# Performance work log

Measured on AMD Instinct MI355X. Metric: run time of the kernel, lower is better.

Reference implementation:

```python
import jax, jax.numpy as jnp
import numpy as np

NEG_SLOPE = 0.2

def setup_inputs() -> dict:
    key = jax.random.key(0)
    ks = jax.random.split(key, 6)
    N, C, H, E_DIM, E = 50000, 128, 64, 16, 800000
    x = jax.random.normal(ks[0], (N, C), dtype=jnp.float32)
    edge_index = jax.random.randint(ks[1], (2, E), 0, N, dtype=jnp.int64)
    edge_attr = jax.random.normal(ks[2], (E, E_DIM), dtype=jnp.float32)
    fc_w = jax.random.normal(ks[3], (H, C), dtype=jnp.float32) * (1.0 / np.sqrt(C))
    fc_b = jnp.zeros((H,), dtype=jnp.float32)
    att_w = jax.random.normal(ks[4], (H, 2 * H + E_DIM), dtype=jnp.float32) * (1.0 / np.sqrt(2 * H + E_DIM))
    att_b = jnp.zeros((H,), dtype=jnp.float32)
    return {"x": x, "edge_index": edge_index, "edge_attr": edge_attr,
            "fc_w": fc_w, "fc_b": fc_b, "att_w": att_w, "att_b": att_b}

def reference(x, edge_index, edge_attr, fc_w, fc_b, att_w, att_b):
    # Node projection: h = fc(x), [N, H]
    h = x @ fc_w.T + fc_b
    src = edge_index[0]  # i (destination of aggregation)
    dst = edge_index[1]  # j (neighbor whose features are aggregated)
    h_i = h[src]                      # [E, H]
    h_j = h[dst]                      # [E, H]
    feat = jnp.concatenate([h_i, h_j, edge_attr], axis=-1)  # [E, 2H+edge_dim]
    alpha = jax.nn.leaky_relu(feat @ att_w.T + att_b, negative_slope=NEG_SLOPE)  # [E, H]
    # dropout is identity in eval mode (training=False)
    msg = h_j * alpha                 # [E, H]
    out = jax.ops.segment_sum(msg, src, num_segments=h.shape[0])  # scatter-add into out[i]
    return out
```

## Files before the change

### kernel.cpp

```cpp
#include <hip/hip_runtime.h>


#define HID 64

__global__ __launch_bounds__(256) void node_kernel(
    const float* __restrict__ x,
    const float* __restrict__ fc_w, const float* __restrict__ fc_b,
    const float* __restrict__ att_w, const float* __restrict__ att_b,
    float* __restrict__ ai_out, float2* __restrict__ hjaj_out, int N)
{
    __shared__ __align__(16) float4 wF[64 * 32];
    __shared__ __align__(16) float4 wI[64 * 16];
    __shared__ __align__(16) float4 wJ[64 * 16];
    __shared__ __align__(16) float xs[4][128];
    __shared__ __align__(16) float hs[4][64];

    const int t = threadIdx.x;
    for (int idx = t; idx < 64 * 32; idx += 256) {
        int l = idx >> 5, c = idx & 31;
        wF[l * 32 + (c ^ (l & 31))] =
            *reinterpret_cast<const float4*>(fc_w + l * 128 + c * 4);
    }
    for (int idx = t; idx < 64 * 16; idx += 256) {
        int l = idx >> 4, c = idx & 15;
        wI[l * 16 + (c ^ (l & 15))] =
            *reinterpret_cast<const float4*>(att_w + l * 144 + c * 4);
        wJ[l * 16 + (c ^ (l & 15))] =
            *reinterpret_cast<const float4*>(att_w + l * 144 + 64 + c * 4);
    }
    __syncthreads();

    const int w = t >> 6, l = t & 63;
    const float bF = fc_b[l];
    const float bA = att_b[l];
    const int waveId = blockIdx.x * 4 + w;
    const int nWaves = gridDim.x * 4;

    for (int n = waveId; n < N; n += nWaves) {
        float2 xv = reinterpret_cast<const float2*>(x)[n * 64 + l];
        xs[w][2 * l] = xv.x;
        xs[w][2 * l + 1] = xv.y;
        float acc = bF;
        #pragma unroll
        for (int c = 0; c < 32; ++c) {
            float4 wv = wF[l * 32 + (c ^ (l & 31))];
            float4 xc = *reinterpret_cast<const float4*>(&xs[w][c * 4]);
            acc = fmaf(wv.x, xc.x, acc);
            acc = fmaf(wv.y, xc.y, acc);
            acc = fmaf(wv.z, xc.z, acc);
            acc = fmaf(wv.w, xc.w, acc);
        }
        hs[w][l] = acc;
        float a2 = bA, a3 = 0.f;
        #pragma unroll
        for (int c = 0; c < 16; ++c) {
            float4 hv = *reinterpret_cast<const float4*>(&hs[w][c * 4]);
            float4 wi = wI[l * 16 + (c ^ (l & 15))];
            float4 wj = wJ[l * 16 + (c ^ (l & 15))];
            a2 = fmaf(wi.x, hv.x, a2); a2 = fmaf(wi.y, hv.y, a2);
            a2 = fmaf(wi.z, hv.z, a2); a2 = fmaf(wi.w, hv.w, a2);
            a3 = fmaf(wj.x, hv.x, a3); a3 = fmaf(wj.y, hv.y, a3);
            a3 = fmaf(wj.z, hv.z, a3); a3 = fmaf(wj.w, hv.w, a3);
        }
        ai_out[n * 64 + l] = a2;
        hjaj_out[n * 64 + l] = make_float2(acc, a3);
    }
}

__global__ __launch_bounds__(256) void edge_kernel(
    const int* __restrict__ ei,
    const float* __restrict__ ea,
    const float* __restrict__ ai,
    const float2* __restrict__ hjaj,
    const float* __restrict__ att_w,
    float* __restrict__ out, int E)
{
    __shared__ __align__(16) float4 eas[4][256];

    const int t = threadIdx.x;
    const int w = t >> 6, l = t & 63;

    float we[16];
    #pragma unroll
    for (int k = 0; k < 16; ++k) we[k] = att_w[l * 144 + 128 + k];

    const int waveId = blockIdx.x * 4 + w;
    const int nWaves = gridDim.x * 4;
    const float4* ea4 = reinterpret_cast<const float4*>(ea);

    for (int e0 = waveId * 64; e0 < E; e0 += nWaves * 64) {
        const int nE = min(64, E - e0);
        int src = 0, dst = 0;
        if (l < nE) {
            src = ei[e0 + l];
            dst = ei[E + e0 + l];
        }
        #pragma unroll
        for (int r = 0; r < 4; ++r) {
            int f = r * 64 + l;
            if (f < nE * 4) eas[w][f] = ea4[(size_t)e0 * 4 + f];
        }
        asm volatile("s_waitcnt lgkmcnt(0)" ::: "memory");

        for (int e = 0; e < nE; ++e) {
            int s = __shfl(src, e);
            int d = __shfl(dst, e);
            float a_src = ai[s * 64 + l];
            float2 hd = hjaj[d * 64 + l];
            float4 v0 = eas[w][e * 4 + 0];
            float4 v1 = eas[w][e * 4 + 1];
            float4 v2 = eas[w][e * 4 + 2];
            float4 v3 = eas[w][e * 4 + 3];
            float pre = a_src + hd.y;
            pre = fmaf(we[0], v0.x, pre);  pre = fmaf(we[1], v0.y, pre);
            pre = fmaf(we[2], v0.z, pre);  pre = fmaf(we[3], v0.w, pre);
            pre = fmaf(we[4], v1.x, pre);  pre = fmaf(we[5], v1.y, pre);
            pre = fmaf(we[6], v1.z, pre);  pre = fmaf(we[7], v1.w, pre);
            pre = fmaf(we[8], v2.x, pre);  pre = fmaf(we[9], v2.y, pre);
            pre = fmaf(we[10], v2.z, pre); pre = fmaf(we[11], v2.w, pre);
            pre = fmaf(we[12], v3.x, pre); pre = fmaf(we[13], v3.y, pre);
            pre = fmaf(we[14], v3.z, pre); pre = fmaf(we[15], v3.w, pre);
            float alpha = pre > 0.f ? pre : 0.2f * pre;
            atomicAdd(&out[(size_t)s * 64 + l], hd.x * alpha);
        }
    }
}

extern "C" void kernel_launch(void* const* d_in, const int* in_sizes, int n_in,
                              void* d_out, int out_size, void* d_ws, size_t ws_size,
                              hipStream_t stream) {
    const float* x     = (const float*)d_in[0];
    const int*   ei    = (const int*)d_in[1];
    const float* ea    = (const float*)d_in[2];
    const float* fc_w  = (const float*)d_in[3];
    const float* fc_b  = (const float*)d_in[4];
    const float* att_w = (const float*)d_in[5];
    const float* att_b = (const float*)d_in[6];
    float* out = (float*)d_out;

    const int N = in_sizes[0] / 128;
    const int E = in_sizes[2] / 16;

    float*  ai   = (float*)d_ws;
    float2* hjaj = (float2*)((char*)d_ws + (size_t)N * 64 * sizeof(float));

    hipMemsetAsync(d_out, 0, (size_t)out_size * sizeof(float), stream);

    node_kernel<<<512, 256, 0, stream>>>(x, fc_w, fc_b, att_w, att_b, ai, hjaj, N);
    edge_kernel<<<1024, 256, 0, stream>>>(ei, ea, ai, hjaj, att_w, out, E);
}
```

Measured before the change: 284.0 us.

## Replace atomic edge scatter with per-node CSR gather and bf16 packed features

Builds a CSR grouping of edges by source node each call: count by histogram, single-block prefix scan, then an atomic-slot scatter that also packs edge attributes to bf16. The edge kernel then gives one wave per node, accumulates messages in registers and writes each output row once, so the output memset and per-edge float atomics go away. Node features h and the j-side attention term are packed as bf16 pairs to halve gather traffic, with 8 gathers batched per step. The cost is the extra build passes, a serial single-block scan, reduced precision, and load imbalance across node degrees.

```diff
diff --git a/kernel.cpp b/kernel.cpp
--- a/kernel.cpp
+++ b/kernel.cpp
@@ -1,13 +1,19 @@
 #include <hip/hip_runtime.h>
 
 
-#define HID 64
+__device__ __forceinline__ unsigned bf16r(float f) {
+    unsigned u = __float_as_uint(f);
+    return (u + 0x7fffu + ((u >> 16) & 1u)) >> 16;
+}
+__device__ __forceinline__ float bf_lo(unsigned p) { return __uint_as_float(p << 16); }
+__device__ __forceinline__ float bf_hi(unsigned p) { return __uint_as_float(p & 0xffff0000u); }
 
 __global__ __launch_bounds__(256) void node_kernel(
     const float* __restrict__ x,
     const float* __restrict__ fc_w, const float* __restrict__ fc_b,
     const float* __restrict__ att_w, const float* __restrict__ att_b,
-    float* __restrict__ ai_out, float2* __restrict__ hjaj_out, int N)
+    const int* __restrict__ ei, int* __restrict__ count,
+    float* __restrict__ ai_out, unsigned* __restrict__ hj_out, int N, int E)
 {
     __shared__ __align__(16) float4 wF[64 * 32];
     __shared__ __align__(16) float4 wI[64 * 16];
@@ -37,7 +43,7 @@
     const int nWaves = gridDim.x * 4;
 
     for (int n = waveId; n < N; n += nWaves) {
-        float2 xv = reinterpret_cast<const float2*>(x)[n * 64 + l];
+        float2 xv = reinterpret_cast<const float2*>(x)[(size_t)n * 64 + l];
         xs[w][2 * l] = xv.x;
         xs[w][2 * l + 1] = xv.y;
         float acc = bF;
@@ -54,76 +60,145 @@
         float a2 = bA, a3 = 0.f;
         #pragma unroll
         for (int c = 0; c < 16; ++c) {
-            float4 hv = *reinterpret_cast<const float4*>(&hs[w][c * 4]);
+            float4 hvv = *reinterpret_cast<const float4*>(&hs[w][c * 4]);
             float4 wi = wI[l * 16 + (c ^ (l & 15))];
             float4 wj = wJ[l * 16 + (c ^ (l & 15))];
-            a2 = fmaf(wi.x, hv.x, a2); a2 = fmaf(wi.y, hv.y, a2);
-            a2 = fmaf(wi.z, hv.z, a2); a2 = fmaf(wi.w, hv.w, a2);
-            a3 = fmaf(wj.x, hv.x, a3); a3 = fmaf(wj.y, hv.y, a3);
-            a3 = fmaf(wj.z, hv.z, a3); a3 = fmaf(wj.w, hv.w, a3);
-        }
-        ai_out[n * 64 + l] = a2;
-        hjaj_out[n * 64 + l] = make_float2(acc, a3);
-    }
-}
-
-__global__ __launch_bounds__(256) void edge_kernel(
-    const int* __restrict__ ei,
-    const float* __restrict__ ea,
-    const float* __restrict__ ai,
-    const float2* __restrict__ hjaj,
-    const float* __restrict__ att_w,
-    float* __restrict__ out, int E)
-{
-    __shared__ __align__(16) float4 eas[4][256];
-
-    const int t = threadIdx.x;
-    const int w = t >> 6, l = t & 63;
+            a2 = fmaf(wi.x, hvv.x, a2); a2 = fmaf(wi.y, hvv.y, a2);
+            a2 = fmaf(wi.z, hvv.z, a2); a2 = fmaf(wi.w, hvv.w, a2);
+            a3 = fmaf(wj.x, hvv.x, a3); a3 = fmaf(wj.y, hvv.y, a3);
+            a3 = fmaf(wj.z, hvv.z, a3); a3 = fmaf(wj.w, hvv.w, a3);
+        }
+        ai_out[(size_t)n * 64 + l] = a2;
+        hj_out[(size_t)n * 64 + l] = (bf16r(a3) << 16) | bf16r(acc);
+    }
+
+    for (int i = blockIdx.x * 256 + t; i < E; i += gridDim.x * 256)
+        atomicAdd(&count[ei[i]], 1);
+}
+
+__global__ __launch_bounds__(1024) void scan_kernel(
+    const int* __restrict__ count, int* __restrict__ start, int N)
+{
+    __shared__ int wsums[16];
+    const int t = threadIdx.x, lane = t & 63, w = t >> 6;
+    int carry = 0;
+    for (int base = 0; base < N; base += 1024) {
+        int i = base + t;
+        int c = (i < N) ? count[i] : 0;
+        int v = c;
+        #pragma unroll
+        for (int off = 1; off < 64; off <<= 1) {
+            int u = __shfl_up(v, off);
+            if (lane >= off) v += u;
+        }
+        if (lane == 63) wsums[w] = v;
+        __syncthreads();
+        int wbase = 0, total = 0;
+        #pragma unroll
+        for (int q = 0; q < 16; ++q) {
+            int s = wsums[q];
+            if (q < w) wbase += s;
+            total += s;
+        }
+        if (i < N) start[i] = carry + wbase + v - c;
+        carry += total;
+        __syncthreads();
+    }
+}
+
+__global__ __launch_bounds__(256) void scatter_kernel(
+    const int* __restrict__ ei, int* __restrict__ start,
+    int* __restrict__ sd, uint4* __restrict__ eaS,
+    const float4* __restrict__ ea4, int E)
+{
+    int i = blockIdx.x * 256 + threadIdx.x;
+    int stride = gridDim.x * 256;
+    for (; i < E; i += stride) {
+        int s = ei[i];
+        int pos = atomicAdd(&start[s], 1);
+        sd[pos] = ei[E + i];
+        float4 r0 = ea4[(size_t)i * 4 + 0], r1 = ea4[(size_t)i * 4 + 1];
+        float4 r2 = ea4[(size_t)i * 4 + 2], r3 = ea4[(size_t)i * 4 + 3];
+        uint4 q0 = make_uint4((bf16r(r0.y) << 16) | bf16r(r0.x),
+                              (bf16r(r0.w) << 16) | bf16r(r0.z),
+                              (bf16r(r1.y) << 16) | bf16r(r1.x),
+                              (bf16r(r1.w) << 16) | bf16r(r1.z));
+        uint4 q1 = make_uint4((bf16r(r2.y) << 16) | bf16r(r2.x),
+                              (bf16r(r2.w) << 16) | bf16r(r2.z),
+                              (bf16r(r3.y) << 16) | bf16r(r3.x),
+                              (bf16r(r3.w) << 16) | bf16r(r3.z));
+        eaS[(size_t)pos * 2 + 0] = q0;
+        eaS[(size_t)pos * 2 + 1] = q1;
+    }
+}
+
+__global__ __launch_bounds__(256) void csr_edge_kernel(
+    const int* __restrict__ sd, const uint2* __restrict__ eaS2,
+    const int* __restrict__ endp, const int* __restrict__ count,
+    const float* __restrict__ ai, const unsigned* __restrict__ hj,
+    const float* __restrict__ att_w, float* __restrict__ out, int N)
+{
+    __shared__ uint2 eas[4][256];
+    __shared__ float weS[64][17];
+
+    const int t = threadIdx.x, w = t >> 6, l = t & 63;
+    for (int idx = t; idx < 1024; idx += 256)
+        weS[idx >> 4][idx & 15] = att_w[(idx >> 4) * 144 + 128 + (idx & 15)];
+    __syncthreads();
+
+    const int n = blockIdx.x * 4 + w;
+    if (n >= N) return;
 
     float we[16];
     #pragma unroll
-    for (int k = 0; k < 16; ++k) we[k] = att_w[l * 144 + 128 + k];
-
-    const int waveId = blockIdx.x * 4 + w;
-    const int nWaves = gridDim.x * 4;
-    const float4* ea4 = reinterpret_cast<const float4*>(ea);
-
-    for (int e0 = waveId * 64; e0 < E; e0 += nWaves * 64) {
-        const int nE = min(64, E - e0);
-        int src = 0, dst = 0;
-        if (l < nE) {
-            src = ei[e0 + l];
-            dst = ei[E + e0 + l];
-        }
-        #pragma unroll
-        for (int r = 0; r < 4; ++r) {
-            int f = r * 64 + l;
-            if (f < nE * 4) eas[w][f] = ea4[(size_t)e0 * 4 + f];
-        }
-        asm volatile("s_waitcnt lgkmcnt(0)" ::: "memory");
-
-        for (int e = 0; e < nE; ++e) {
-            int s = __shfl(src, e);
-            int d = __shfl(dst, e);
-            float a_src = ai[s * 64 + l];
-            float2 hd = hjaj[d * 64 + l];
-            float4 v0 = eas[w][e * 4 + 0];
-            float4 v1 = eas[w][e * 4 + 1];
-            float4 v2 = eas[w][e * 4 + 2];
-            float4 v3 = eas[w][e * 4 + 3];
-            float pre = a_src + hd.y;
-            pre = fmaf(we[0], v0.x, pre);  pre = fmaf(we[1], v0.y, pre);
-            pre = fmaf(we[2], v0.z, pre);  pre = fmaf(we[3], v0.w, pre);
-            pre = fmaf(we[4], v1.x, pre);  pre = fmaf(we[5], v1.y, pre);
-            pre = fmaf(we[6], v1.z, pre);  pre = fmaf(we[7], v1.w, pre);
-            pre = fmaf(we[8], v2.x, pre);  pre = fmaf(we[9], v2.y, pre);
-            pre = fmaf(we[10], v2.z, pre); pre = fmaf(we[11], v2.w, pre);
-            pre = fmaf(we[12], v3.x, pre); pre = fmaf(we[13], v3.y, pre);
-            pre = fmaf(we[14], v3.z, pre); pre = fmaf(we[15], v3.w, pre);
-            float alpha = pre > 0.f ? pre : 0.2f * pre;
-            atomicAdd(&out[(size_t)s * 64 + l], hd.x * alpha);
-        }
-    }
+    for (int k = 0; k < 16; ++k) we[k] = weS[l][k];
+
+    const int deg = count[n];
+    const int base = endp[n] - deg;
+    const float aiv = ai[(size_t)n * 64 + l];
+    float acc = 0.f;
+
+#define EDGE_BODY(KK, UU)                                                      \
+    {                                                                          \
+        float pre = aiv + bf_hi(UU);                                           \
+        _Pragma("unroll") for (int r = 0; r < 4; ++r) {                        \
+            uint2 q = eas[w][(KK) * 4 + r];                                    \
+            pre = fmaf(we[r * 4 + 0], bf_lo(q.x), pre);                        \
+            pre = fmaf(we[r * 4 + 1], bf_hi(q.x), pre);                        \
+            pre = fmaf(we[r * 4 + 2], bf_lo(q.y), pre);                        \
+            pre = fmaf(we[r * 4 + 3], bf_hi(q.y), pre);                        \
+        }                                                                      \
+        float alpha = pre > 0.f ? pre : 0.2f * pre;                            \
+        acc = fmaf(bf_lo(UU), alpha, acc);                                     \
+    }
+
+    int done = 0;
+    while (done < deg) {
+        const int rem = min(64, deg - done);
+        int v = 0;
+        if (l < rem) v = sd[base + done + l];
+        for (int f = l; f < rem * 4; f += 64)
+            eas[w][f] = eaS2[(size_t)(base + done) * 4 + f];
+        int k = 0;
+        for (; k + 8 <= rem; k += 8) {
+            int d[8]; unsigned u[8];
+            #pragma unroll
+            for (int j = 0; j < 8; ++j) {
+                d[j] = __shfl(v, k + j);
+                u[j] = hj[(size_t)d[j] * 64 + l];
+            }
+            #pragma unroll
+            for (int j = 0; j < 8; ++j) EDGE_BODY(k + j, u[j]);
+        }
+        for (; k < rem; ++k) {
+            int dd = __shfl(v, k);
+            unsigned uu = hj[(size_t)dd * 64 + l];
+            EDGE_BODY(k, uu);
+        }
+        done += rem;
+    }
+#undef EDGE_BODY
+    out[(size_t)n * 64 + l] = acc;
 }
 
 extern "C" void kernel_launch(void* const* d_in, const int* in_sizes, int n_in,
@@ -141,11 +216,22 @@
     const int N = in_sizes[0] / 128;
     const int E = in_sizes[2] / 16;
 
-    float*  ai   = (float*)d_ws;
-    float2* hjaj = (float2*)((char*)d_ws + (size_t)N * 64 * sizeof(float));
-
-    hipMemsetAsync(d_out, 0, (size_t)out_size * sizeof(float), stream);
-
-    node_kernel<<<512, 256, 0, stream>>>(x, fc_w, fc_b, att_w, att_b, ai, hjaj, N);
-    edge_kernel<<<1024, 256, 0, stream>>>(ei, ea, ai, hjaj, att_w, out, E);
-}
+    char* p = (char*)d_ws;
+    auto align256 = [](size_t v) { return (v + 255) & ~(size_t)255; };
+    float*    ai    = (float*)p;        p += align256((size_t)N * 64 * 4);
+    unsigned* hj    = (unsigned*)p;     p += align256((size_t)N * 64 * 4);
+    int*      count = (int*)p;          p += align256((size_t)N * 4);
+    int*      startp= (int*)p;          p += align256((size_t)N * 4);
+    int*      sd    = (int*)p;          p += align256((size_t)E * 4);
+    uint4*    eaS   = (uint4*)p;
+
+    hipMemsetAsync(count, 0, (size_t)N * sizeof(int), stream);
+
+    node_kernel<<<512, 256, 0, stream>>>(x, fc_w, fc_b, att_w, att_b,
+                                         ei, count, ai, hj, N, E);
+    scan_kernel<<<1, 1024, 0, stream>>>(count, startp, N);
+    scatter_kernel<<<1024, 256, 0, stream>>>(ei, startp, sd, eaS,
+                                             (const float4*)ea, E);
+    csr_edge_kernel<<<(N + 3) / 4, 256, 0, stream>>>(
+        sd, (const uint2*)eaS, startp, count, ai, hj, att_w, out, N);
+}
```

Result: faster. 254.2 us (-10.5%).
